# Optimization experiments

Hardware: AMD Instinct MI355X
Metric: run time of the kernel (lower is better)

The kernel has to match this reference:

```python
import jax, jax.numpy as jnp
import numpy as np
import math

UNIT = 46
KEY_SIZE = 16
MAX_POS = 50
NEG_BIG = 1.0e12


def _rope_tables(max_pos, d):
    pos = np.arange(max_pos, dtype=np.float32)[:, None]
    div = np.exp(np.arange(0, d, 2, dtype=np.float32) * (-math.log(10000.0) / d))
    sin = np.sin(pos * div)  # [P, d/2]
    cos = np.cos(pos * div)  # [P, d/2]
    # matches torch repeat_interleave(2, dim=-1) of the strided sinusoid table
    cos_rep = np.repeat(cos, 2, axis=-1)  # [P, d]
    sin_rep = np.repeat(sin, 2, axis=-1)  # [P, d]
    return jnp.asarray(cos_rep), jnp.asarray(sin_rep)

_COS, _SIN = _rope_tables(MAX_POS, KEY_SIZE)


def _apply_rope(qw):
    # qw: [B, S, d]
    s = qw.shape[-2]
    qw2 = jnp.stack([-qw[..., 1::2], qw[..., ::2]], axis=-1).reshape(qw.shape)
    return qw * _COS[:s] + qw2 * _SIN[:s]


def setup_inputs() -> dict:
    key = jax.random.key(0)
    ks = jax.random.split(key, 8)
    B, S = 32768, 50
    x = jax.random.normal(ks[0], (B, S, UNIT), dtype=jnp.float32)
    mask = jnp.ones((B, S), dtype=jnp.float32)
    d_in = UNIT
    sc = 1.0 / math.sqrt(d_in)
    Wi = jax.random.uniform(ks[1], (2 * UNIT + KEY_SIZE, d_in), minval=-sc, maxval=sc, dtype=jnp.float32)
    bi = jax.random.uniform(ks[2], (2 * UNIT + KEY_SIZE,), minval=-sc, maxval=sc, dtype=jnp.float32)
    Wo = jax.random.uniform(ks[3], (UNIT, UNIT), minval=-sc, maxval=sc, dtype=jnp.float32)
    bo = jax.random.uniform(ks[4], (UNIT,), minval=-sc, maxval=sc, dtype=jnp.float32)
    Wq = jax.random.uniform(ks[5], (1, UNIT), minval=-sc, maxval=sc, dtype=jnp.float32)
    bq = jax.random.uniform(ks[6], (1,), minval=-sc, maxval=sc, dtype=jnp.float32)
    scale_q = jnp.ones((KEY_SIZE,), jnp.float32)
    offset_q = jnp.zeros((KEY_SIZE,), jnp.float32)
    scale_k = jnp.ones((KEY_SIZE,), jnp.float32)
    offset_k = jnp.zeros((KEY_SIZE,), jnp.float32)
    return {"x": x, "mask": mask, "Wi": Wi, "bi": bi, "Wo": Wo, "bo": bo,
            "scale_q": scale_q, "offset_q": offset_q, "scale_k": scale_k,
            "offset_k": offset_k, "Wq": Wq, "bq": bq}


def reference(x, mask, Wi, bi, Wo, bo, scale_q, offset_q, scale_k, offset_k, Wq, bq):
    # x: [B, S, U], mask: [B, S]
    h = jax.nn.silu(jnp.einsum('bsu,ou->bso', x, Wi) + bi)  # [B, S, 2U+K]
    u, v, qk = jnp.split(h, [UNIT, 2 * UNIT], axis=-1)
    q = _apply_rope(qk * scale_q + offset_q)  # [B, S, K]
    k = _apply_rope(qk * scale_k + offset_k)  # [B, S, K]
    A = jnp.einsum('bik,bjk->bij', q, k) / math.sqrt(KEY_SIZE)  # [B, S, S]
    m = mask[:, None, :]
    A = jax.nn.softmax(A * m + (1.0 - m) * (-NEG_BIG), axis=-1)
    # NOTE: original overwrites the gated output with a plain matmul (u unused)
    out = jnp.einsum('bij,bju->biu', A, v)  # [B, S, U]
    out = jnp.einsum('biu,ou->bio', out, Wo) + bo  # [B, S, U]
    prob = (jnp.einsum('bsu,ou->bso', out, Wq) + bq)[..., 0]  # [B, S]
    prob = prob * mask - (1.0 - mask) * NEG_BIG
    prob = jax.nn.softmax(prob, axis=-1)
    return jnp.sum(out * prob[..., None], axis=1)  # [B, U]
```

## Files before the change

kernel.cpp:

```cpp
#include <hip/hip_runtime.h>
#include <math.h>

#define SEQ 50
#define UNITD 46
#define NEGBIG 1000000000000.0f

typedef _Float16 f16;
typedef f16 f16x4 __attribute__((ext_vector_type(4)));
typedef f16 f16x8 __attribute__((ext_vector_type(8)));
typedef float f32x4 __attribute__((ext_vector_type(4)));
typedef unsigned u32x2 __attribute__((ext_vector_type(2)));
typedef unsigned u32x4 __attribute__((ext_vector_type(4)));

__device__ __forceinline__ float rcpf(float x) { return __builtin_amdgcn_rcpf(x); }
__device__ __forceinline__ unsigned pk2(float lo, float hi) {
    return __builtin_bit_cast(unsigned, __builtin_amdgcn_cvt_pkrtz(lo, hi));
}

template<int CTRL>
__device__ __forceinline__ float dmov(float x) {
    int v = __builtin_bit_cast(int, x);
    return __builtin_bit_cast(float, __builtin_amdgcn_update_dpp(v, v, CTRL, 0xF, 0xF, true));
}
__device__ __forceinline__ float dsum16(float x) {
    x += dmov<0xB1>(x);
    x += dmov<0x4E>(x);
    x += dmov<0x141>(x);
    x += dmov<0x140>(x);
    return x;
}
__device__ __forceinline__ float dmax16(float x) {
    x = fmaxf(x, dmov<0xB1>(x));  x = fmaxf(x, dmov<0x4E>(x));
    x = fmaxf(x, dmov<0x141>(x)); x = fmaxf(x, dmov<0x140>(x));
    return x;
}

#define ARENA 12800
#define QOFF 0
#define KOFF 2560
#define VOFF 6400
#define MOFF 12544

__device__ __forceinline__ int swzP(int row, int colbyte) {
    return row * 128 + (colbyte ^ ((row & 7) << 4));
}
__device__ __forceinline__ int swzV(int row, int colbyte) {
    return VOFF + row * 128 + (colbyte ^ ((row & 7) << 4));
}

#define WS_ROPE 14336

__global__ void prep_kernel(const float* __restrict__ Wi,
                            const float* __restrict__ Wo,
                            char* __restrict__ ws)
{
    f16x8* wf = (f16x8*)ws;
    const int lane = threadIdx.x & 63;
    const int g = lane >> 4, t = lane & 15;
    #pragma unroll
    for (int nt = 0; nt < 4; ++nt) {
        int c = t + 16 * nt; bool cok = c < 62;
        const float* wr = Wi + (size_t)(UNITD + (cok ? c : 0)) * UNITD;
        #pragma unroll
        for (int kt = 0; kt < 2; ++kt) {
            f16x8 f;
            #pragma unroll
            for (int jj = 0; jj < 8; ++jj) {
                int u = 32 * kt + 8 * g + jj;
                f[jj] = (f16)((cok && u < UNITD) ? wr[u] : 0.f);
            }
            wf[(nt * 2 + kt) * 64 + lane] = f;
        }
    }
    #pragma unroll
    for (int mo = 0; mo < 3; ++mo) {
        int o = 16 * mo + t; bool ook = o < UNITD;
        const float* wr = Wo + (size_t)(ook ? o : 0) * UNITD;
        #pragma unroll
        for (int kt = 0; kt < 2; ++kt) {
            f16x8 f;
            #pragma unroll
            for (int jj = 0; jj < 8; ++jj) {
                int u = 32 * kt + 8 * g + jj;
                f[jj] = (f16)((ook && u < UNITD) ? wr[u] : 0.f);
            }
            wf[512 + (mo * 2 + kt) * 64 + lane] = f;
        }
    }
    {
        float2* rt = (float2*)(ws + WS_ROPE);
        int seq = threadIdx.x;
        #pragma unroll
        for (int d = 0; d < 16; ++d) {
            float ang = (float)seq * expf(-(float)(d >> 1) * 1.1512925464970229f);
            float sn, cs;
            sincosf(ang, &sn, &cs);
            float2 v; v.x = cs * 0.5f; v.y = ((d & 1) ? sn : -sn) * 0.5f;
            rt[seq * 16 + d] = v;
        }
    }
}

__global__ __launch_bounds__(256, 3) void gau_kernel(
    const float* __restrict__ x,
    const float* __restrict__ mask,
    const char* __restrict__ ws,
    const float* __restrict__ bi,
    const float* __restrict__ bo,
    const float* __restrict__ sq,
    const float* __restrict__ oq,
    const float* __restrict__ sk,
    const float* __restrict__ ok,
    const float* __restrict__ Wq,
    const float* __restrict__ bq,
    float* __restrict__ out,
    int Btot)
{
    const int lane = threadIdx.x & 63;
    const int wid  = threadIdx.x >> 6;
    const int b    = blockIdx.x * 4 + wid;
    const int g    = lane >> 4;
    const int t    = lane & 15;

    const f16x8* wf = (const f16x8*)ws;

    __shared__ __align__(16) char smem[4 * ARENA];
    char* wa = smem + wid * ARENA;
    float* M = (float*)(wa + MOFF);

    if (b >= Btot) return;

    M[lane] = (lane < SEQ) ? mask[(size_t)b * SEQ + lane] : 0.f;

    f16x8 bfW[4][2];
    float biv[4];
    #pragma unroll
    for (int nt = 0; nt < 4; ++nt) {
        int c = t + 16 * nt;
        biv[nt] = (c < 62) ? bi[UNITD + c] : 0.f;
        #pragma unroll
        for (int kt = 0; kt < 2; ++kt)
            bfW[nt][kt] = wf[(nt * 2 + kt) * 64 + lane];
    }

    f32x4 hB[4][4];
    #pragma unroll
    for (int mt = 0; mt < 4; ++mt)
        #pragma unroll
        for (int nt = 0; nt < 4; ++nt) {
            f32x4 c; c[0] = biv[nt]; c[1] = biv[nt]; c[2] = biv[nt]; c[3] = biv[nt];
            hB[mt][nt] = c;
        }

    const float* xb = x + (size_t)b * (SEQ * UNITD);
    #pragma unroll
    for (int mt = 0; mt < 4; ++mt) {
        int row = 16 * mt + t; if (row > SEQ - 1) row = SEQ - 1;
        const float* xr = xb + row * UNITD;
        #pragma unroll
        for (int kt = 0; kt < 2; ++kt) {
            u32x4 axw;
            #pragma unroll
            for (int jj2 = 0; jj2 < 4; ++jj2) {
                int u = 32 * kt + 8 * g + 2 * jj2;
                float lo = 0.f, hi = 0.f;
                if (u < UNITD) { float2 w = *(const float2*)(xr + u); lo = w.x; hi = w.y; }
                axw[jj2] = pk2(lo, hi);
            }
            f16x8 ax = __builtin_bit_cast(f16x8, axw);
            #pragma unroll
            for (int nt = 0; nt < 4; ++nt)
                hB[mt][nt] = __builtin_amdgcn_mfma_f32_16x16x32_f16(ax, bfW[nt][kt], hB[mt][nt], 0, 0, 0);
        }
    }

    float qkv[4][4];
    #pragma unroll
    for (int mt = 0; mt < 4; ++mt) {
        float s2[4], s3[4];
        #pragma unroll
        for (int nt = 0; nt < 4; ++nt) {
            float sl[4];
            #pragma unroll
            for (int r = 0; r < 4; ++r) {
                float h = hB[mt][nt][r];
                sl[r] = h * rcpf(1.f + __expf(-h));
            }
            int ucol = t + 16 * nt;
            if (nt < 3 && ucol < UNITD) {
                u32x2 pw; pw[0] = pk2(sl[0], sl[1]); pw[1] = pk2(sl[2], sl[3]);
                *(f16x4*)(wa + swzV(ucol, (16 * mt + 4 * g) * 2)) = __builtin_bit_cast(f16x4, pw);
            }
            if (nt == 2) { s2[0]=sl[0]; s2[1]=sl[1]; s2[2]=sl[2]; s2[3]=sl[3]; }
            if (nt == 3) { s3[0]=sl[0]; s3[1]=sl[1]; s3[2]=sl[2]; s3[3]=sl[3]; }
        }
        #pragma unroll
        for (int r = 0; r < 4; ++r) qkv[mt][r] = (t >= 14) ? s2[r] : s3[r];
    }

    {
        f16* Q = (f16*)(wa + QOFF);
        f16* K = (f16*)(wa + KOFF);
        const float2* rt = (const float2*)(ws + WS_ROPE);
        int d = (t >= 14) ? (t - 14) : (t + 2);
        float sqd = sq[d], oqd = oq[d], skd = sk[d], okd = ok[d];
        #pragma unroll
        for (int mt = 0; mt < 4; ++mt)
            #pragma unroll
            for (int r = 0; r < 4; ++r) {
                int seq = 16 * mt + 4 * g + r;
                float2 cn = rt[seq * 16 + d];
                float qv = qkv[mt][r] * sqd + oqd;
                float kv = qkv[mt][r] * skd + okd;
                float qp = dmov<0xB1>(qv);
                float kp = dmov<0xB1>(kv);
                Q[seq * 20 + d] = (f16)(qv * cn.x + qp * cn.y);
                K[seq * 20 + d] = (f16)(kv * cn.x + kp * cn.y);
            }
    }

    f16x4 ak[4], bq_[4];
    #pragma unroll
    for (int m4 = 0; m4 < 4; ++m4) ak[m4]  = *(f16x4*)(wa + KOFF + (16 * m4 + t) * 40 + 8 * g);
    #pragma unroll
    for (int n4 = 0; n4 < 4; ++n4) bq_[n4] = *(f16x4*)(wa + QOFF + (16 * n4 + t) * 40 + 8 * g);

    f32x4 pT[4][4];
    #pragma unroll
    for (int m4 = 0; m4 < 4; ++m4)
        #pragma unroll
        for (int n4 = 0; n4 < 4; ++n4) {
            f32x4 z; z[0]=0.f; z[1]=0.f; z[2]=0.f; z[3]=0.f;
            pT[m4][n4] = __builtin_amdgcn_mfma_f32_16x16x16f16(ak[m4], bq_[n4], z, 0, 0, 0);
        }

    f32x4 mj4[4];
    float NBv[4][4];
    #pragma unroll
    for (int m4 = 0; m4 < 4; ++m4) {
        mj4[m4] = *(f32x4*)(M + 16 * m4 + 4 * g);
        #pragma unroll
        for (int r = 0; r < 4; ++r)
            NBv[m4][r] = fmaf(mj4[m4][r], NEGBIG, -NEGBIG);
    }

    #pragma unroll
    for (int n4 = 0; n4 < 4; ++n4) {
        float a_[4][4];
        #pragma unroll
        for (int m4 = 0; m4 < 4; ++m4)
            #pragma unroll
            for (int r = 0; r < 4; ++r)
                a_[m4][r] = fmaf(pT[m4][n4][r], mj4[m4][r], NBv[m4][r]);

        float mr[4];
        #pragma unroll
        for (int m4 = 0; m4 < 4; ++m4)
            mr[m4] = fmaxf(fmaxf(a_[m4][0], a_[m4][1]), fmaxf(a_[m4][2], a_[m4][3]));
        float mx = fmaxf(fmaxf(mr[0], mr[1]), fmaxf(mr[2], mr[3]));
        mx = fmaxf(mx, __shfl_xor(mx, 16)); mx = fmaxf(mx, __shfl_xor(mx, 32));

        float sr[4];
        #pragma unroll
        for (int m4 = 0; m4 < 4; ++m4) {
            #pragma unroll
            for (int r = 0; r < 4; ++r) a_[m4][r] = __expf(a_[m4][r] - mx);
            sr[m4] = (a_[m4][0] + a_[m4][1]) + (a_[m4][2] + a_[m4][3]);
        }
        float sm = (sr[0] + sr[1]) + (sr[2] + sr[3]);
        sm += __shfl_xor(sm, 16); sm += __shfl_xor(sm, 32);
        float inv = rcpf(sm);

        int i = t + 16 * n4;
        if (i < SEQ) {
            #pragma unroll
            for (int m4 = 0; m4 < 4; ++m4) {
                u32x2 pw;
                pw[0] = pk2(a_[m4][0] * inv, a_[m4][1] * inv);
                pw[1] = pk2(a_[m4][2] * inv, a_[m4][3] * inv);
                *(f16x4*)(wa + swzP(i, (16 * m4 + 4 * g) * 2)) = __builtin_bit_cast(f16x4, pw);
            }
        }
    }

    f16x8 bv[3][2];
    #pragma unroll
    for (int nt = 0; nt < 3; ++nt)
        #pragma unroll
        for (int kt = 0; kt < 2; ++kt)
            bv[nt][kt] = *(f16x8*)(wa + swzV(t + 16 * nt, (32 * kt + 8 * g) * 2));

    f32x4 oA[4][3];
    #pragma unroll
    for (int mt = 0; mt < 4; ++mt)
        #pragma unroll
        for (int nt = 0; nt < 3; ++nt) { f32x4 z; z[0]=0.f; z[1]=0.f; z[2]=0.f; z[3]=0.f; oA[mt][nt] = z; }

    #pragma unroll
    for (int mt = 0; mt < 4; ++mt) {
        int pr = 16 * mt + t; if (pr > SEQ - 1) pr = SEQ - 1;
        #pragma unroll
        for (int kt = 0; kt < 2; ++kt) {
            f16x8 ap = *(f16x8*)(wa + swzP(pr, (32 * kt + 8 * g) * 2));
            #pragma unroll
            for (int nt = 0; nt < 3; ++nt)
                oA[mt][nt] = __builtin_amdgcn_mfma_f32_16x16x32_f16(ap, bv[nt][kt], oA[mt][nt], 0, 0, 0);
        }
    }

    #pragma unroll
    for (int mt = 0; mt < 4; ++mt)
        #pragma unroll
        for (int nt = 0; nt < 3; ++nt) {
            int u = t + 16 * nt;
            if (u < UNITD) {
                #pragma unroll
                for (int r = 0; r < 4; ++r) {
                    int i = 4 * g + r + 16 * mt;
                    if (i < SEQ)
                        *(f16*)(wa + swzP(i, u * 2)) = (f16)oA[mt][nt][r];
                }
            }
        }

    f16x8 aw[3][2];
    #pragma unroll
    for (int mo = 0; mo < 3; ++mo)
        #pragma unroll
        for (int kt = 0; kt < 2; ++kt)
            aw[mo][kt] = wf[512 + (mo * 2 + kt) * 64 + lane];

    float bov[3][4], wqv[3][4];
    #pragma unroll
    for (int mo = 0; mo < 3; ++mo)
        #pragma unroll
        for (int r = 0; r < 4; ++r) {
            int o = 16 * mo + 4 * g + r; bool ok2 = (o < UNITD);
            bov[mo][r] = ok2 ? bo[o] : 0.f;
            wqv[mo][r] = ok2 ? Wq[o] : 0.f;
        }

    f32x4 o2[3][4];
    #pragma unroll
    for (int mo = 0; mo < 3; ++mo)
        #pragma unroll
        for (int n4 = 0; n4 < 4; ++n4) {
            f32x4 c;
            #pragma unroll
            for (int r = 0; r < 4; ++r) c[r] = bov[mo][r];
            o2[mo][n4] = c;
        }

    #pragma unroll
    for (int n4 = 0; n4 < 4; ++n4) {
        int br = t + 16 * n4; if (br > SEQ - 1) br = SEQ - 1;
        #pragma unroll
        for (int kt = 0; kt < 2; ++kt) {
            f16x8 bo_ = *(f16x8*)(wa + swzP(br, (32 * kt + 8 * g) * 2));
            #pragma unroll
            for (int mo = 0; mo < 3; ++mo)
                o2[mo][n4] = __builtin_amdgcn_mfma_f32_16x16x32_f16(aw[mo][kt], bo_, o2[mo][n4], 0, 0, 0);
        }
    }

    float bq0 = bq[0];
    float tv[4]; float mx2 = -INFINITY;
    #pragma unroll
    for (int n4 = 0; n4 < 4; ++n4) {
        float s = 0.f;
        #pragma unroll
        for (int mo = 0; mo < 3; ++mo)
            #pragma unroll
            for (int r = 0; r < 4; ++r) s += o2[mo][n4][r] * wqv[mo][r];
        s += __shfl_xor(s, 16); s += __shfl_xor(s, 32);
        float mi = M[t + 16 * n4];
        float nb = fmaf(mi, NEGBIG, -NEGBIG);
        tv[n4] = fmaf(s + bq0, mi, nb);
        mx2 = fmaxf(mx2, tv[n4]);
    }
    mx2 = dmax16(mx2);
    float sm2 = 0.f;
    #pragma unroll
    for (int n4 = 0; n4 < 4; ++n4) { float e = __expf(tv[n4] - mx2); tv[n4] = e; sm2 += e; }
    sm2 = dsum16(sm2);
    float inv2 = rcpf(sm2);

    #pragma unroll
    for (int mo = 0; mo < 3; ++mo) {
        float racc[4];
        #pragma unroll
        for (int r = 0; r < 4; ++r) {
            float a = 0.f;
            #pragma unroll
            for (int n4 = 0; n4 < 4; ++n4) a += o2[mo][n4][r] * tv[n4];
            racc[r] = dsum16(a);
        }
        if (t == 0) {
            #pragma unroll
            for (int r = 0; r < 4; ++r) {
                int o = 16 * mo + 4 * g + r;
                if (o < UNITD) out[(size_t)b * UNITD + o] = racc[r] * inv2;
            }
        }
    }
}

extern "C" void kernel_launch(void* const* d_in, const int* in_sizes, int n_in,
                              void* d_out, int out_size, void* d_ws, size_t ws_size,
                              hipStream_t stream) {
    const float* x    = (const float*)d_in[0];
    const float* mask = (const float*)d_in[1];
    const float* Wi   = (const float*)d_in[2];
    const float* bi   = (const float*)d_in[3];
    const float* Wo   = (const float*)d_in[4];
    const float* bo   = (const float*)d_in[5];
    const float* sq   = (const float*)d_in[6];
    const float* oq   = (const float*)d_in[7];
    const float* sk   = (const float*)d_in[8];
    const float* ok   = (const float*)d_in[9];
    const float* Wq   = (const float*)d_in[10];
    const float* bq   = (const float*)d_in[11];
    float* outp       = (float*)d_out;

    prep_kernel<<<1, 64, 0, stream>>>(Wi, Wo, (char*)d_ws);

    const int B = in_sizes[0] / (SEQ * UNITD);
    const int blocks = (B + 3) / 4;
    gau_kernel<<<blocks, 256, 0, stream>>>(x, mask, (const char*)d_ws, bi, bo,
                                           sq, oq, sk, ok, Wq, bq, outp, B);
}
```

Baseline: 173.1 us.

## Keep softmax probabilities and PV output in registers, skip LDS round-trips

```diff
diff --git a/kernel.cpp b/kernel.cpp
--- a/kernel.cpp
+++ b/kernel.cpp
@@ -23,10 +23,8 @@
     return __builtin_bit_cast(float, __builtin_amdgcn_update_dpp(v, v, CTRL, 0xF, 0xF, true));
 }
 __device__ __forceinline__ float dsum16(float x) {
-    x += dmov<0xB1>(x);
-    x += dmov<0x4E>(x);
-    x += dmov<0x141>(x);
-    x += dmov<0x140>(x);
+    x += dmov<0xB1>(x);  x += dmov<0x4E>(x);
+    x += dmov<0x141>(x); x += dmov<0x140>(x);
     return x;
 }
 __device__ __forceinline__ float dmax16(float x) {
@@ -41,13 +39,11 @@
 #define VOFF 6400
 #define MOFF 12544
 
-__device__ __forceinline__ int swzP(int row, int colbyte) {
-    return row * 128 + (colbyte ^ ((row & 7) << 4));
-}
 __device__ __forceinline__ int swzV(int row, int colbyte) {
     return VOFF + row * 128 + (colbyte ^ ((row & 7) << 4));
 }
 
+#define WS_WO   8192
 #define WS_ROPE 14336
 
 __global__ void prep_kernel(const float* __restrict__ Wi,
@@ -55,6 +51,7 @@
                             char* __restrict__ ws)
 {
     f16x8* wf = (f16x8*)ws;
+    u32x2* wo2 = (u32x2*)(ws + WS_WO);
     const int lane = threadIdx.x & 63;
     const int g = lane >> 4, t = lane & 15;
     #pragma unroll
@@ -77,14 +74,15 @@
         int o = 16 * mo + t; bool ook = o < UNITD;
         const float* wr = Wo + (size_t)(ook ? o : 0) * UNITD;
         #pragma unroll
-        for (int kt = 0; kt < 2; ++kt) {
-            f16x8 f;
-            #pragma unroll
-            for (int jj = 0; jj < 8; ++jj) {
-                int u = 32 * kt + 8 * g + jj;
-                f[jj] = (f16)((ook && u < UNITD) ? wr[u] : 0.f);
-            }
-            wf[512 + (mo * 2 + kt) * 64 + lane] = f;
+        for (int kt2 = 0; kt2 < 3; ++kt2) {
+            float v[4];
+            #pragma unroll
+            for (int jj = 0; jj < 4; ++jj) {
+                int u = 16 * kt2 + 4 * g + jj;
+                v[jj] = (ook && u < UNITD) ? wr[u] : 0.f;
+            }
+            u32x2 f; f[0] = pk2(v[0], v[1]); f[1] = pk2(v[2], v[3]);
+            wo2[(mo * 3 + kt2) * 64 + lane] = f;
         }
     }
     {
@@ -123,6 +121,7 @@
     const int t    = lane & 15;
 
     const f16x8* wf = (const f16x8*)ws;
+    const u32x2* wo2 = (const u32x2*)(ws + WS_WO);
 
     __shared__ __align__(16) char smem[4 * ARENA];
     char* wa = smem + wid * ARENA;
@@ -244,6 +243,7 @@
             NBv[m4][r] = fmaf(mj4[m4][r], NEGBIG, -NEGBIG);
     }
 
+    f16x4 pb[4][4];
     #pragma unroll
     for (int n4 = 0; n4 < 4; ++n4) {
         float a_[4][4];
@@ -271,64 +271,32 @@
         sm += __shfl_xor(sm, 16); sm += __shfl_xor(sm, 32);
         float inv = rcpf(sm);
 
-        int i = t + 16 * n4;
-        if (i < SEQ) {
-            #pragma unroll
-            for (int m4 = 0; m4 < 4; ++m4) {
-                u32x2 pw;
-                pw[0] = pk2(a_[m4][0] * inv, a_[m4][1] * inv);
-                pw[1] = pk2(a_[m4][2] * inv, a_[m4][3] * inv);
-                *(f16x4*)(wa + swzP(i, (16 * m4 + 4 * g) * 2)) = __builtin_bit_cast(f16x4, pw);
-            }
-        }
-    }
-
-    f16x8 bv[3][2];
+        #pragma unroll
+        for (int m4 = 0; m4 < 4; ++m4) {
+            u32x2 pw;
+            pw[0] = pk2(a_[m4][0] * inv, a_[m4][1] * inv);
+            pw[1] = pk2(a_[m4][2] * inv, a_[m4][3] * inv);
+            pb[n4][m4] = __builtin_bit_cast(f16x4, pw);
+        }
+    }
+
+    f32x4 oT[3][4];
     #pragma unroll
     for (int nt = 0; nt < 3; ++nt)
         #pragma unroll
-        for (int kt = 0; kt < 2; ++kt)
-            bv[nt][kt] = *(f16x8*)(wa + swzV(t + 16 * nt, (32 * kt + 8 * g) * 2));
-
-    f32x4 oA[4][3];
-    #pragma unroll
-    for (int mt = 0; mt < 4; ++mt)
-        #pragma unroll
-        for (int nt = 0; nt < 3; ++nt) { f32x4 z; z[0]=0.f; z[1]=0.f; z[2]=0.f; z[3]=0.f; oA[mt][nt] = z; }
-
-    #pragma unroll
-    for (int mt = 0; mt < 4; ++mt) {
-        int pr = 16 * mt + t; if (pr > SEQ - 1) pr = SEQ - 1;
-        #pragma unroll
-        for (int kt = 0; kt < 2; ++kt) {
-            f16x8 ap = *(f16x8*)(wa + swzP(pr, (32 * kt + 8 * g) * 2));
-            #pragma unroll
-            for (int nt = 0; nt < 3; ++nt)
-                oA[mt][nt] = __builtin_amdgcn_mfma_f32_16x16x32_f16(ap, bv[nt][kt], oA[mt][nt], 0, 0, 0);
-        }
-    }
-
-    #pragma unroll
-    for (int mt = 0; mt < 4; ++mt)
-        #pragma unroll
-        for (int nt = 0; nt < 3; ++nt) {
-            int u = t + 16 * nt;
-            if (u < UNITD) {
-                #pragma unroll
-                for (int r = 0; r < 4; ++r) {
-                    int i = 4 * g + r + 16 * mt;
-                    if (i < SEQ)
-                        *(f16*)(wa + swzP(i, u * 2)) = (f16)oA[mt][nt][r];
-                }
-            }
-        }
-
-    f16x8 aw[3][2];
-    #pragma unroll
-    for (int mo = 0; mo < 3; ++mo)
-        #pragma unroll
-        for (int kt = 0; kt < 2; ++kt)
-            aw[mo][kt] = wf[512 + (mo * 2 + kt) * 64 + lane];
+        for (int n4 = 0; n4 < 4; ++n4) { f32x4 z; z[0]=0.f; z[1]=0.f; z[2]=0.f; z[3]=0.f; oT[nt][n4] = z; }
+
+    #pragma unroll
+    for (int nt = 0; nt < 3; ++nt) {
+        int vr = t + 16 * nt; if (vr > UNITD - 1) vr = UNITD - 1;
+        #pragma unroll
+        for (int m4 = 0; m4 < 4; ++m4) {
+            f16x4 av = *(f16x4*)(wa + swzV(vr, (16 * m4 + 4 * g) * 2));
+            #pragma unroll
+            for (int n4 = 0; n4 < 4; ++n4)
+                oT[nt][n4] = __builtin_amdgcn_mfma_f32_16x16x16f16(av, pb[n4][m4], oT[nt][n4], 0, 0, 0);
+        }
+    }
 
     float bov[3][4], wqv[3][4];
     #pragma unroll
@@ -352,14 +320,20 @@
         }
 
     #pragma unroll
-    for (int n4 = 0; n4 < 4; ++n4) {
-        int br = t + 16 * n4; if (br > SEQ - 1) br = SEQ - 1;
-        #pragma unroll
-        for (int kt = 0; kt < 2; ++kt) {
-            f16x8 bo_ = *(f16x8*)(wa + swzP(br, (32 * kt + 8 * g) * 2));
+    for (int kt2 = 0; kt2 < 3; ++kt2) {
+        f16x4 awf[3];
+        #pragma unroll
+        for (int mo = 0; mo < 3; ++mo)
+            awf[mo] = __builtin_bit_cast(f16x4, wo2[(mo * 3 + kt2) * 64 + lane]);
+        #pragma unroll
+        for (int n4 = 0; n4 < 4; ++n4) {
+            u32x2 bw;
+            bw[0] = pk2(oT[kt2][n4][0], oT[kt2][n4][1]);
+            bw[1] = pk2(oT[kt2][n4][2], oT[kt2][n4][3]);
+            f16x4 bof = __builtin_bit_cast(f16x4, bw);
             #pragma unroll
             for (int mo = 0; mo < 3; ++mo)
-                o2[mo][n4] = __builtin_amdgcn_mfma_f32_16x16x32_f16(aw[mo][kt], bo_, o2[mo][n4], 0, 0, 0);
+                o2[mo][n4] = __builtin_amdgcn_mfma_f32_16x16x16f16(awf[mo], bof, o2[mo][n4], 0, 0, 0);
         }
     }
 
```

Result: faster. 168.3 us, median of 2 (-2.8%).
